# Kernel tuning notes

Measured on AMD Instinct MI355X. Metric: run time of the kernel, lower is better.

Reference implementation:

```python
import jax, jax.numpy as jnp
import numpy as np

STRIDES = (8, 16, 32, 64, 128)
SCORE_THR = 0.05
IOU_THR = 0.6
MAX_NUM = 150
USE_CTR = True
B, NC = 64, 20
HW = (128, 64, 32, 16, 8)


def _reshape(feat):
    # [B,C,H,W] -> [B,H*W,C]
    b, c, h, w = feat.shape
    return feat.transpose(0, 2, 3, 1).reshape(b, h * w, c)


def _decode(feat, stride):
    # feat: [B,4,H,W] reg offsets; returns [B,HW,4] boxes (x1,y1,x2,y2)
    _, _, h, w = feat.shape
    xs = jnp.arange(w, dtype=jnp.float32) * stride + (stride // 2)
    ys = jnp.arange(h, dtype=jnp.float32) * stride + (stride // 2)
    yy, xx = jnp.meshgrid(ys, xs, indexing='ij')
    coords = jnp.stack([xx.reshape(-1), yy.reshape(-1)], axis=-1)  # [HW,2]
    off = _reshape(feat) * stride  # [B,HW,4]
    xy1 = coords[None] - off[..., :2]
    xy2 = coords[None] + off[..., 2:]
    return jnp.concatenate([xy1, xy2], axis=-1)


def _nms_single(scores, ids, boxes, valid):
    # scores already sorted descending (from top_k); class-aware offset NMS.
    coord_max = jnp.max(jnp.where(valid[:, None], boxes, -jnp.inf))
    coord_max = jnp.where(jnp.isfinite(coord_max), coord_max, 0.0)
    ob = boxes + (ids.astype(boxes.dtype) * (coord_max + 1.0))[:, None]
    x1, y1, x2, y2 = ob[:, 0], ob[:, 1], ob[:, 2], ob[:, 3]
    areas = (x2 - x1 + 1.0) * (y2 - y1 + 1.0)
    xmin = jnp.maximum(x1[:, None], x1[None, :])
    ymin = jnp.maximum(y1[:, None], y1[None, :])
    xmax = jnp.minimum(x2[:, None], x2[None, :])
    ymax = jnp.minimum(y2[:, None], y2[None, :])
    ow = jnp.clip(xmax - xmin, 0.0)
    oh = jnp.clip(ymax - ymin, 0.0)
    overlap = ow * oh
    union = jnp.clip(areas[:, None] + areas[None, :] - overlap, 1e-10)
    iou = overlap / union  # [N,N]
    n = scores.shape[0]
    idx = jnp.arange(n)

    def body(i, keep):
        sup = keep[i] & (iou[i] > IOU_THR) & (idx > i)
        return keep & ~sup

    return jax.lax.fori_loop(0, n, body, valid)


def setup_inputs() -> dict:
    key = jax.random.key(0)
    ks = jax.random.split(key, 15)
    out = {}
    for li, hw in enumerate(HW):
        out[f'cls{li}'] = jax.random.normal(ks[li], (B, NC, hw, hw), jnp.float32)
        out[f'reg{li}'] = jax.random.uniform(ks[5 + li], (B, 4, hw, hw), jnp.float32)
        out[f'ctr{li}'] = jax.random.normal(ks[10 + li], (B, 1, hw, hw), jnp.float32)
    return out


def reference(cls0, cls1, cls2, cls3, cls4,
              reg0, reg1, reg2, reg3, reg4,
              ctr0, ctr1, ctr2, ctr3, ctr4):
    cls_feats = (cls0, cls1, cls2, cls3, cls4)
    reg_feats = (reg0, reg1, reg2, reg3, reg4)
    ctr_feats = (ctr0, ctr1, ctr2, ctr3, ctr4)

    cls_logits = jnp.concatenate([_reshape(f) for f in cls_feats], axis=1)  # [B,A,NC]
    ctr_logits = jnp.concatenate([_reshape(f) for f in ctr_feats], axis=1)  # [B,A,1]
    cls_preds = jax.nn.sigmoid(cls_logits)
    ctr_preds = jax.nn.sigmoid(ctr_logits)

    cls_scores = jnp.max(cls_preds, axis=-1)  # [B,A]
    cls_ids = jnp.argmax(cls_preds, axis=-1) + 1  # [B,A]
    if USE_CTR:
        cls_scores = jnp.sqrt(cls_scores * ctr_preds[..., 0])

    boxes = jnp.concatenate(
        [_decode(f, s) for f, s in zip(reg_feats, STRIDES)], axis=1)  # [B,A,4]

    top_scores, top_idx = jax.lax.top_k(cls_scores, MAX_NUM)  # sorted desc
    top_ids = jnp.take_along_axis(cls_ids, top_idx, axis=1)
    top_boxes = jnp.take_along_axis(boxes, top_idx[..., None], axis=1)

    valid = top_scores > SCORE_THR
    keep = jax.vmap(_nms_single)(top_scores, top_ids, top_boxes, valid)

    out_scores = jnp.where(keep, top_scores, 0.0)
    out_ids = jnp.where(keep, top_ids, 0)
    out_boxes = jnp.where(keep[..., None], top_boxes, 0.0)
    return out_scores, out_ids, out_boxes, keep
```

## Files before the change

### kernel.cpp

```cpp
#include <hip/hip_runtime.h>
#include <cstdint>
#include <cstddef>

#define NPTS 21824
#define NB   64
#define NCLS 20
#define MAXN 150
#define NCHUNK 11
#define CHSZ 2048

typedef unsigned long long u64;
typedef unsigned int u32;


__device__ __forceinline__ u64 radix_select_top(
    const u64* __restrict__ keys, int n, int k0,
    u32* hist, u32* suf, u64* shp, int* shr, int* shb)
{
    int tid = threadIdx.x;
    if (tid == 0) { *shp = 0ull; *shr = k0; }
    __syncthreads();
    for (int pass = 0; pass < 6; ++pass) {
        int sh = 56 - pass * 8;
        hist[tid] = 0u;
        __syncthreads();
        u64 prefix = *shp;
        int r = *shr;
        for (int i = tid; i < n; i += 256) {
            u64 key = keys[i];
            bool ok = (pass == 0) || ((key >> (sh + 8)) == prefix);
            if (ok) atomicAdd(&hist[(u32)(key >> sh) & 255u], 1u);
        }
        __syncthreads();
        suf[tid] = hist[tid];
        __syncthreads();
        for (int d = 1; d < 256; d <<= 1) {
            u32 v = (tid + d < 256) ? suf[tid + d] : 0u;
            __syncthreads();
            suf[tid] += v;
            __syncthreads();
        }
        u32 nxt = (tid == 255) ? 0u : suf[tid + 1];
        if (suf[tid] >= (u32)r && nxt < (u32)r) {
            *shb = tid;
            *shr = r - (int)nxt;
        }
        __syncthreads();
        if (tid == 0) *shp = (prefix << 8) | (u64)(u32)(*shb);
        __syncthreads();
    }
    u64 T = (*shp) << 16;
    __syncthreads();
    return T;
}

__global__ __launch_bounds__(256) void k_part(
    const float* __restrict__ c0, const float* __restrict__ c1,
    const float* __restrict__ c2, const float* __restrict__ c3,
    const float* __restrict__ c4,
    const float* __restrict__ t0, const float* __restrict__ t1,
    const float* __restrict__ t2, const float* __restrict__ t3,
    const float* __restrict__ t4,
    u64* __restrict__ cand)
{
    __shared__ u64 keys[CHSZ];
    __shared__ u32 hist[256], suf[256];
    __shared__ u64 shp; __shared__ int shr, shb, shcnt;

    const int tid   = threadIdx.x;
    const int chunk = blockIdx.x;
    const int b     = blockIdx.y;
    const int cbase = chunk * CHSZ;

    for (int half = 0; half < 2; ++half) {
        int pl = half * 1024 + tid * 4;
        int p  = cbase + pl;
        u64 kk0 = 0, kk1 = 0, kk2 = 0, kk3 = 0;
        if (p < NPTS) {
            const float* cp; const float* tp; int base; size_t hw;
            if (p < 16384)      { cp = c0; tp = t0; base = 0;     hw = 16384; }
            else if (p < 20480) { cp = c1; tp = t1; base = 16384; hw = 4096;  }
            else if (p < 21504) { cp = c2; tp = t2; base = 20480; hw = 1024;  }
            else if (p < 21760) { cp = c3; tp = t3; base = 21504; hw = 256;   }
            else                { cp = c4; tp = t4; base = 21760; hw = 64;    }
            int q = p - base;
            const float* cb = cp + (size_t)b * NCLS * hw + q;

            float best0 = -1.f, best1 = -1.f, best2 = -1.f, best3 = -1.f;
            int   bi0 = 0, bi1 = 0, bi2 = 0, bi3 = 0;
            for (int c = 0; c < NCLS; ++c) {
                const float4 v = *reinterpret_cast<const float4*>(cb + (size_t)c * hw);
                float sg;
                sg = 1.0f / (1.0f + expf(-v.x)); if (sg > best0) { best0 = sg; bi0 = c; }
                sg = 1.0f / (1.0f + expf(-v.y)); if (sg > best1) { best1 = sg; bi1 = c; }
                sg = 1.0f / (1.0f + expf(-v.z)); if (sg > best2) { best2 = sg; bi2 = c; }
                sg = 1.0f / (1.0f + expf(-v.w)); if (sg > best3) { best3 = sg; bi3 = c; }
            }
            const float4 cv = *reinterpret_cast<const float4*>(tp + (size_t)b * hw + q);
            float sct, sc;
            sct = 1.0f / (1.0f + expf(-cv.x)); sc = sqrtf(__fmul_rn(best0, sct));
            kk0 = ((u64)__float_as_uint(sc) << 32) | ((u64)(u32)(21823 - p)     << 17) | ((u64)(u32)(bi0 + 1) << 12);
            sct = 1.0f / (1.0f + expf(-cv.y)); sc = sqrtf(__fmul_rn(best1, sct));
            kk1 = ((u64)__float_as_uint(sc) << 32) | ((u64)(u32)(21823 - (p+1)) << 17) | ((u64)(u32)(bi1 + 1) << 12);
            sct = 1.0f / (1.0f + expf(-cv.z)); sc = sqrtf(__fmul_rn(best2, sct));
            kk2 = ((u64)__float_as_uint(sc) << 32) | ((u64)(u32)(21823 - (p+2)) << 17) | ((u64)(u32)(bi2 + 1) << 12);
            sct = 1.0f / (1.0f + expf(-cv.w)); sc = sqrtf(__fmul_rn(best3, sct));
            kk3 = ((u64)__float_as_uint(sc) << 32) | ((u64)(u32)(21823 - (p+3)) << 17) | ((u64)(u32)(bi3 + 1) << 12);
        }
        keys[pl + 0] = kk0; keys[pl + 1] = kk1;
        keys[pl + 2] = kk2; keys[pl + 3] = kk3;
    }
    __syncthreads();

    u64 T = radix_select_top(keys, CHSZ, MAXN, hist, suf, &shp, &shr, &shb);
    if (tid == 0) shcnt = 0;
    __syncthreads();

    u64* outp = cand + ((size_t)b * NCHUNK + chunk) * MAXN;
    for (int i = tid; i < CHSZ; i += 256) {
        u64 key = keys[i];
        if (key >= T) {
            int pos = atomicAdd(&shcnt, 1);
            if (pos < MAXN) outp[pos] = key;
        }
    }
}

__global__ __launch_bounds__(256) void k_final(
    const float* __restrict__ r0, const float* __restrict__ r1,
    const float* __restrict__ r2, const float* __restrict__ r3,
    const float* __restrict__ r4,
    const u64* __restrict__ cand,
    float* __restrict__ out)
{
    const int NC2 = NCHUNK * MAXN;
    __shared__ u64 ck[NCHUNK * MAXN];
    __shared__ u32 hist[256], suf[256];
    __shared__ u64 shp; __shared__ int shr, shb, shcnt;
    __shared__ u64 win[MAXN], srt[MAXN];
    __shared__ float bx0[MAXN], bx1[MAXN], bx2[MAXN], bx3[MAXN];
    __shared__ float ox1[MAXN], oy1[MAXN], ox2[MAXN], oy2[MAXN], area[MAXN];
    __shared__ float sc[MAXN];
    __shared__ int   idv[MAXN];
    __shared__ u64 sup[MAXN][3];
    __shared__ u64 keepw[3];
    __shared__ float shcmax;
    __shared__ float wmax[4];

    const int b = blockIdx.x, tid = threadIdx.x;

    for (int i = tid; i < NC2; i += 256) ck[i] = cand[(size_t)b * NC2 + i];
    __syncthreads();

    u64 T = radix_select_top(ck, NC2, MAXN, hist, suf, &shp, &shr, &shb);
    if (tid == 0) shcnt = 0;
    __syncthreads();
    for (int i = tid; i < NC2; i += 256) {
        u64 key = ck[i];
        if (key >= T) {
            int pos = atomicAdd(&shcnt, 1);
            if (pos < MAXN) win[pos] = key;
        }
    }
    __syncthreads();

    if (tid < MAXN) {
        u64 mk = win[tid]; int r = 0;
        for (int j = 0; j < MAXN; ++j) r += (win[j] > mk);
        srt[r] = mk;
    }
    __syncthreads();

    if (tid < MAXN) {
        u64 key = srt[tid];
        sc[tid]  = __uint_as_float((u32)(key >> 32));
        int p    = 21823 - (int)((key >> 17) & 0x7FFFu);
        idv[tid] = (int)((key >> 12) & 31u);

        const float* rp; int base, dim, lg, st;
        if (p < 16384)      { rp = r0; base = 0;     dim = 128; lg = 7; st = 8;   }
        else if (p < 20480) { rp = r1; base = 16384; dim = 64;  lg = 6; st = 16;  }
        else if (p < 21504) { rp = r2; base = 20480; dim = 32;  lg = 5; st = 32;  }
        else if (p < 21760) { rp = r3; base = 21504; dim = 16;  lg = 4; st = 64;  }
        else                { rp = r4; base = 21760; dim = 8;   lg = 3; st = 128; }

        int q = p - base;
        int y = q >> lg;
        int x = q & (dim - 1);
        float s  = (float)st;
        float cx = (float)(x * st + (st >> 1));
        float cy = (float)(y * st + (st >> 1));
        size_t hw = (size_t)dim * dim;
        const float* rg = rp + (size_t)b * 4 * hw + q;
        float a0 = rg[0], a1 = rg[hw], a2 = rg[2 * hw], a3 = rg[3 * hw];
        bx0[tid] = __fsub_rn(cx, __fmul_rn(a0, s));
        bx1[tid] = __fsub_rn(cy, __fmul_rn(a1, s));
        bx2[tid] = __fadd_rn(cx, __fmul_rn(a2, s));
        bx3[tid] = __fadd_rn(cy, __fmul_rn(a3, s));
    }
    __syncthreads();

    float m = -INFINITY;
    if (tid < MAXN && sc[tid] > 0.05f)
        m = fmaxf(fmaxf(bx0[tid], bx1[tid]), fmaxf(bx2[tid], bx3[tid]));
    #pragma unroll
    for (int off = 32; off >= 1; off >>= 1) m = fmaxf(m, __shfl_xor(m, off));
    if ((tid & 63) == 0) wmax[tid >> 6] = m;
    __syncthreads();
    if (tid == 0) {
        float mm = fmaxf(fmaxf(wmax[0], wmax[1]), fmaxf(wmax[2], wmax[3]));
        shcmax = isfinite(mm) ? mm : 0.0f;
    }
    __syncthreads();

    float cm1 = __fadd_rn(shcmax, 1.0f);
    if (tid < MAXN) {
        float off = __fmul_rn((float)idv[tid], cm1);
        float X1 = __fadd_rn(bx0[tid], off);
        float Y1 = __fadd_rn(bx1[tid], off);
        float X2 = __fadd_rn(bx2[tid], off);
        float Y2 = __fadd_rn(bx3[tid], off);
        ox1[tid] = X1; oy1[tid] = Y1; ox2[tid] = X2; oy2[tid] = Y2;
        area[tid] = __fmul_rn(__fadd_rn(__fsub_rn(X2, X1), 1.0f),
                              __fadd_rn(__fsub_rn(Y2, Y1), 1.0f));
    }
    __syncthreads();

    for (int t = tid; t < MAXN * 3; t += 256) {
        int i = t / 3;
        int w = t - i * 3;
        float x1i = ox1[i], y1i = oy1[i], x2i = ox2[i], y2i = oy2[i], ai = area[i];
        u64 bits = 0ull;
        for (int e = 0; e < 64; ++e) {
            int j = w * 64 + e;
            if (j >= MAXN) break;
            float xmin = fmaxf(x1i, ox1[j]);
            float ymin = fmaxf(y1i, oy1[j]);
            float xmax = fminf(x2i, ox2[j]);
            float ymax = fminf(y2i, oy2[j]);
            float ow = fmaxf(__fsub_rn(xmax, xmin), 0.0f);
            float oh = fmaxf(__fsub_rn(ymax, ymin), 0.0f);
            float ov = __fmul_rn(ow, oh);
            float un = fmaxf(__fsub_rn(__fadd_rn(ai, area[j]), ov), 1e-10f);
            float iou = __fdiv_rn(ov, un);
            if (iou > 0.6f) bits |= (1ull << e);
        }
        sup[i][w] = bits;
    }
    __syncthreads();

    if (tid == 0) {
        u64 kw0 = 0, kw1 = 0, kw2 = 0;
        for (int k = 0; k < MAXN; ++k) {
            if (sc[k] > 0.05f) {
                if (k < 64)       kw0 |= 1ull << k;
                else if (k < 128) kw1 |= 1ull << (k - 64);
                else              kw2 |= 1ull << (k - 128);
            }
        }
        u64 s0 = sup[0][0], s1 = sup[0][1], s2 = sup[0][2];
        for (int i = 0; i < MAXN; ++i) {
            u64 n0 = 0, n1 = 0, n2 = 0;
            if (i + 1 < MAXN) { n0 = sup[i+1][0]; n1 = sup[i+1][1]; n2 = sup[i+1][2]; }
            bool kept = (i < 64) ? ((kw0 >> i) & 1ull)
                      : (i < 128) ? ((kw1 >> (i - 64)) & 1ull)
                                  : ((kw2 >> (i - 128)) & 1ull);
            if (kept) {
                u64 a0, a1, a2;
                if (i < 63)        { a0 = ~((1ull << (i + 1)) - 1ull); a1 = ~0ull; a2 = ~0ull; }
                else if (i == 63)  { a0 = 0ull; a1 = ~0ull; a2 = ~0ull; }
                else if (i < 127)  { a0 = 0ull; a1 = ~((1ull << (i - 63)) - 1ull); a2 = ~0ull; }
                else if (i == 127) { a0 = 0ull; a1 = 0ull; a2 = ~0ull; }
                else               { a0 = 0ull; a1 = 0ull; a2 = ~((1ull << (i - 127)) - 1ull); }
                kw0 &= ~(s0 & a0); kw1 &= ~(s1 & a1); kw2 &= ~(s2 & a2);
            }
            s0 = n0; s1 = n1; s2 = n2;
        }
        keepw[0] = kw0; keepw[1] = kw1; keepw[2] = kw2;
    }
    __syncthreads();

    if (tid < MAXN) {
        bool kp = (keepw[tid >> 6] >> (tid & 63)) & 1ull;
        int o = b * MAXN + tid;
        float* oSc = out;
        float* oId = out + NB * MAXN;
        float* oBx = out + 2 * NB * MAXN;
        float* oKp = out + 2 * NB * MAXN + NB * MAXN * 4;
        oSc[o] = kp ? sc[tid] : 0.0f;
        oId[o] = kp ? (float)idv[tid] : 0.0f;
        oBx[o * 4 + 0] = kp ? bx0[tid] : 0.0f;
        oBx[o * 4 + 1] = kp ? bx1[tid] : 0.0f;
        oBx[o * 4 + 2] = kp ? bx2[tid] : 0.0f;
        oBx[o * 4 + 3] = kp ? bx3[tid] : 0.0f;
        oKp[o] = kp ? 1.0f : 0.0f;
    }
}

extern "C" void kernel_launch(void* const* d_in, const int* in_sizes, int n_in,
                              void* d_out, int out_size, void* d_ws, size_t ws_size,
                              hipStream_t stream)
{
    const float* cls[5]; const float* reg[5]; const float* ctr[5];
    for (int li = 0; li < 5; ++li) {
        cls[li] = (const float*)d_in[3 * li + 0];
        reg[li] = (const float*)d_in[3 * li + 1];
        ctr[li] = (const float*)d_in[3 * li + 2];
    }

    u64* cand = (u64*)d_ws;

    dim3 g1(NCHUNK, NB);
    k_part<<<g1, 256, 0, stream>>>(cls[0], cls[1], cls[2], cls[3], cls[4],
                                   ctr[0], ctr[1], ctr[2], ctr[3], ctr[4],
                                   cand);
    k_final<<<NB, 256, 0, stream>>>(reg[0], reg[1], reg[2], reg[3], reg[4],
                                    cand, (float*)d_out);
}
```

Measured before the change: 287.9 us.

## Replace radix select with bitonic sort and defer argmax to final kernel

Swaps the 6-pass radix-select top-k in both kernels for a shared-memory bitonic sort of 2048 keys, with larger thread blocks (512 and 1024). The class argmax leaves the per-point loop: k_part keeps only the minimum of exp(-x), which is monotone with the max sigmoid, and k_final recomputes the argmax for just the 150 winners. The serial single-thread NMS keep-mask loop becomes a wavefront using shuffles, and the initial valid mask is built with ballot. The bitonic sort does more compare-exchange work and many barriers, but it removes the atomic histograms and the per-element divides.

```diff
diff --git a/kernel.cpp b/kernel.cpp
--- a/kernel.cpp
+++ b/kernel.cpp
@@ -13,48 +13,27 @@
 typedef unsigned int u32;
 
 
-__device__ __forceinline__ u64 radix_select_top(
-    const u64* __restrict__ keys, int n, int k0,
-    u32* hist, u32* suf, u64* shp, int* shr, int* shb)
-{
-    int tid = threadIdx.x;
-    if (tid == 0) { *shp = 0ull; *shr = k0; }
-    __syncthreads();
-    for (int pass = 0; pass < 6; ++pass) {
-        int sh = 56 - pass * 8;
-        hist[tid] = 0u;
-        __syncthreads();
-        u64 prefix = *shp;
-        int r = *shr;
-        for (int i = tid; i < n; i += 256) {
-            u64 key = keys[i];
-            bool ok = (pass == 0) || ((key >> (sh + 8)) == prefix);
-            if (ok) atomicAdd(&hist[(u32)(key >> sh) & 255u], 1u);
-        }
-        __syncthreads();
-        suf[tid] = hist[tid];
-        __syncthreads();
-        for (int d = 1; d < 256; d <<= 1) {
-            u32 v = (tid + d < 256) ? suf[tid + d] : 0u;
+template<int T>
+__device__ __forceinline__ void bitonic2048_desc(u64* keys)
+{
+    const int tid = threadIdx.x;
+    for (int k = 2; k <= 2048; k <<= 1) {
+        for (int j = k >> 1; j > 0; j >>= 1) {
             __syncthreads();
-            suf[tid] += v;
-            __syncthreads();
-        }
-        u32 nxt = (tid == 255) ? 0u : suf[tid + 1];
-        if (suf[tid] >= (u32)r && nxt < (u32)r) {
-            *shb = tid;
-            *shr = r - (int)nxt;
-        }
-        __syncthreads();
-        if (tid == 0) *shp = (prefix << 8) | (u64)(u32)(*shb);
-        __syncthreads();
-    }
-    u64 T = (*shp) << 16;
-    __syncthreads();
-    return T;
-}
-
-__global__ __launch_bounds__(256) void k_part(
+            #pragma unroll
+            for (int t = tid; t < 1024; t += T) {
+                int i = ((t & ~(j - 1)) << 1) | (t & (j - 1));
+                int pr = i | j;
+                u64 a = keys[i], c = keys[pr];
+                bool desc = ((i & k) == 0);
+                if (desc ? (a < c) : (a > c)) { keys[i] = c; keys[pr] = a; }
+            }
+        }
+    }
+    __syncthreads();
+}
+
+__global__ __launch_bounds__(512) void k_part(
     const float* __restrict__ c0, const float* __restrict__ c1,
     const float* __restrict__ c2, const float* __restrict__ c3,
     const float* __restrict__ c4,
@@ -64,69 +43,59 @@
     u64* __restrict__ cand)
 {
     __shared__ u64 keys[CHSZ];
-    __shared__ u32 hist[256], suf[256];
-    __shared__ u64 shp; __shared__ int shr, shb, shcnt;
-
     const int tid   = threadIdx.x;
     const int chunk = blockIdx.x;
     const int b     = blockIdx.y;
-    const int cbase = chunk * CHSZ;
-
-    for (int half = 0; half < 2; ++half) {
-        int pl = half * 1024 + tid * 4;
-        int p  = cbase + pl;
-        u64 kk0 = 0, kk1 = 0, kk2 = 0, kk3 = 0;
-        if (p < NPTS) {
-            const float* cp; const float* tp; int base; size_t hw;
-            if (p < 16384)      { cp = c0; tp = t0; base = 0;     hw = 16384; }
-            else if (p < 20480) { cp = c1; tp = t1; base = 16384; hw = 4096;  }
-            else if (p < 21504) { cp = c2; tp = t2; base = 20480; hw = 1024;  }
-            else if (p < 21760) { cp = c3; tp = t3; base = 21504; hw = 256;   }
-            else                { cp = c4; tp = t4; base = 21760; hw = 64;    }
-            int q = p - base;
-            const float* cb = cp + (size_t)b * NCLS * hw + q;
-
-            float best0 = -1.f, best1 = -1.f, best2 = -1.f, best3 = -1.f;
-            int   bi0 = 0, bi1 = 0, bi2 = 0, bi3 = 0;
-            for (int c = 0; c < NCLS; ++c) {
-                const float4 v = *reinterpret_cast<const float4*>(cb + (size_t)c * hw);
-                float sg;
-                sg = 1.0f / (1.0f + expf(-v.x)); if (sg > best0) { best0 = sg; bi0 = c; }
-                sg = 1.0f / (1.0f + expf(-v.y)); if (sg > best1) { best1 = sg; bi1 = c; }
-                sg = 1.0f / (1.0f + expf(-v.z)); if (sg > best2) { best2 = sg; bi2 = c; }
-                sg = 1.0f / (1.0f + expf(-v.w)); if (sg > best3) { best3 = sg; bi3 = c; }
-            }
-            const float4 cv = *reinterpret_cast<const float4*>(tp + (size_t)b * hw + q);
-            float sct, sc;
-            sct = 1.0f / (1.0f + expf(-cv.x)); sc = sqrtf(__fmul_rn(best0, sct));
-            kk0 = ((u64)__float_as_uint(sc) << 32) | ((u64)(u32)(21823 - p)     << 17) | ((u64)(u32)(bi0 + 1) << 12);
-            sct = 1.0f / (1.0f + expf(-cv.y)); sc = sqrtf(__fmul_rn(best1, sct));
-            kk1 = ((u64)__float_as_uint(sc) << 32) | ((u64)(u32)(21823 - (p+1)) << 17) | ((u64)(u32)(bi1 + 1) << 12);
-            sct = 1.0f / (1.0f + expf(-cv.z)); sc = sqrtf(__fmul_rn(best2, sct));
-            kk2 = ((u64)__float_as_uint(sc) << 32) | ((u64)(u32)(21823 - (p+2)) << 17) | ((u64)(u32)(bi2 + 1) << 12);
-            sct = 1.0f / (1.0f + expf(-cv.w)); sc = sqrtf(__fmul_rn(best3, sct));
-            kk3 = ((u64)__float_as_uint(sc) << 32) | ((u64)(u32)(21823 - (p+3)) << 17) | ((u64)(u32)(bi3 + 1) << 12);
-        }
-        keys[pl + 0] = kk0; keys[pl + 1] = kk1;
-        keys[pl + 2] = kk2; keys[pl + 3] = kk3;
-    }
-    __syncthreads();
-
-    u64 T = radix_select_top(keys, CHSZ, MAXN, hist, suf, &shp, &shr, &shb);
-    if (tid == 0) shcnt = 0;
-    __syncthreads();
-
-    u64* outp = cand + ((size_t)b * NCHUNK + chunk) * MAXN;
-    for (int i = tid; i < CHSZ; i += 256) {
-        u64 key = keys[i];
-        if (key >= T) {
-            int pos = atomicAdd(&shcnt, 1);
-            if (pos < MAXN) outp[pos] = key;
-        }
-    }
-}
-
-__global__ __launch_bounds__(256) void k_final(
+
+    const int pl = tid * 4;
+    const int p  = chunk * CHSZ + pl;
+    u64 kk0 = 0, kk1 = 0, kk2 = 0, kk3 = 0;
+    if (p < NPTS) {
+        const float* cp; const float* tp; int base; size_t hw;
+        if (p < 16384)      { cp = c0; tp = t0; base = 0;     hw = 16384; }
+        else if (p < 20480) { cp = c1; tp = t1; base = 16384; hw = 4096;  }
+        else if (p < 21504) { cp = c2; tp = t2; base = 20480; hw = 1024;  }
+        else if (p < 21760) { cp = c3; tp = t3; base = 21504; hw = 256;   }
+        else                { cp = c4; tp = t4; base = 21760; hw = 64;    }
+        int q = p - base;
+        const float* cb = cp + (size_t)b * NCLS * hw + q;
+
+        float u0 = INFINITY, u1 = INFINITY, u2 = INFINITY, u3 = INFINITY;
+        for (int c = 0; c < NCLS; ++c) {
+            const float4 v = *reinterpret_cast<const float4*>(cb + (size_t)c * hw);
+            u0 = fminf(u0, expf(-v.x));
+            u1 = fminf(u1, expf(-v.y));
+            u2 = fminf(u2, expf(-v.z));
+            u3 = fminf(u3, expf(-v.w));
+        }
+        const float4 cv = *reinterpret_cast<const float4*>(tp + (size_t)b * hw + q);
+        float best, sct, sc;
+        best = 1.0f / (1.0f + u0); sct = 1.0f / (1.0f + expf(-cv.x));
+        sc = sqrtf(__fmul_rn(best, sct));
+        kk0 = ((u64)__float_as_uint(sc) << 32) | (u32)(21823 - p);
+        best = 1.0f / (1.0f + u1); sct = 1.0f / (1.0f + expf(-cv.y));
+        sc = sqrtf(__fmul_rn(best, sct));
+        kk1 = ((u64)__float_as_uint(sc) << 32) | (u32)(21823 - (p + 1));
+        best = 1.0f / (1.0f + u2); sct = 1.0f / (1.0f + expf(-cv.z));
+        sc = sqrtf(__fmul_rn(best, sct));
+        kk2 = ((u64)__float_as_uint(sc) << 32) | (u32)(21823 - (p + 2));
+        best = 1.0f / (1.0f + u3); sct = 1.0f / (1.0f + expf(-cv.w));
+        sc = sqrtf(__fmul_rn(best, sct));
+        kk3 = ((u64)__float_as_uint(sc) << 32) | (u32)(21823 - (p + 3));
+    }
+    keys[pl + 0] = kk0; keys[pl + 1] = kk1;
+    keys[pl + 2] = kk2; keys[pl + 3] = kk3;
+
+    bitonic2048_desc<512>(keys);
+
+    if (tid < MAXN)
+        cand[((size_t)b * NCHUNK + chunk) * MAXN + tid] = keys[tid];
+}
+
+__global__ __launch_bounds__(1024) void k_final(
+    const float* __restrict__ c0, const float* __restrict__ c1,
+    const float* __restrict__ c2, const float* __restrict__ c3,
+    const float* __restrict__ c4,
     const float* __restrict__ r0, const float* __restrict__ r1,
     const float* __restrict__ r2, const float* __restrict__ r3,
     const float* __restrict__ r4,
@@ -134,10 +103,7 @@
     float* __restrict__ out)
 {
     const int NC2 = NCHUNK * MAXN;
-    __shared__ u64 ck[NCHUNK * MAXN];
-    __shared__ u32 hist[256], suf[256];
-    __shared__ u64 shp; __shared__ int shr, shb, shcnt;
-    __shared__ u64 win[MAXN], srt[MAXN];
+    __shared__ u64 keys[CHSZ];
     __shared__ float bx0[MAXN], bx1[MAXN], bx2[MAXN], bx3[MAXN];
     __shared__ float ox1[MAXN], oy1[MAXN], ox2[MAXN], oy2[MAXN], area[MAXN];
     __shared__ float sc[MAXN];
@@ -145,52 +111,44 @@
     __shared__ u64 sup[MAXN][3];
     __shared__ u64 keepw[3];
     __shared__ float shcmax;
-    __shared__ float wmax[4];
+    __shared__ float wmax[16];
 
     const int b = blockIdx.x, tid = threadIdx.x;
 
-    for (int i = tid; i < NC2; i += 256) ck[i] = cand[(size_t)b * NC2 + i];
-    __syncthreads();
-
-    u64 T = radix_select_top(ck, NC2, MAXN, hist, suf, &shp, &shr, &shb);
-    if (tid == 0) shcnt = 0;
-    __syncthreads();
-    for (int i = tid; i < NC2; i += 256) {
-        u64 key = ck[i];
-        if (key >= T) {
-            int pos = atomicAdd(&shcnt, 1);
-            if (pos < MAXN) win[pos] = key;
-        }
-    }
-    __syncthreads();
+    for (int i = tid; i < CHSZ; i += 1024)
+        keys[i] = (i < NC2) ? cand[(size_t)b * NC2 + i] : 0ull;
+
+    bitonic2048_desc<1024>(keys);
 
     if (tid < MAXN) {
-        u64 mk = win[tid]; int r = 0;
-        for (int j = 0; j < MAXN; ++j) r += (win[j] > mk);
-        srt[r] = mk;
-    }
-    __syncthreads();
-
-    if (tid < MAXN) {
-        u64 key = srt[tid];
-        sc[tid]  = __uint_as_float((u32)(key >> 32));
-        int p    = 21823 - (int)((key >> 17) & 0x7FFFu);
-        idv[tid] = (int)((key >> 12) & 31u);
-
-        const float* rp; int base, dim, lg, st;
-        if (p < 16384)      { rp = r0; base = 0;     dim = 128; lg = 7; st = 8;   }
-        else if (p < 20480) { rp = r1; base = 16384; dim = 64;  lg = 6; st = 16;  }
-        else if (p < 21504) { rp = r2; base = 20480; dim = 32;  lg = 5; st = 32;  }
-        else if (p < 21760) { rp = r3; base = 21504; dim = 16;  lg = 4; st = 64;  }
-        else                { rp = r4; base = 21760; dim = 8;   lg = 3; st = 128; }
+        u64 key = keys[tid];
+        sc[tid] = __uint_as_float((u32)(key >> 32));
+        int p   = 21823 - (int)(key & 0x7FFFu);
+
+        const float* rp; const float* cp; int base, dim, lg, st;
+        if (p < 16384)      { rp = r0; cp = c0; base = 0;     dim = 128; lg = 7; st = 8;   }
+        else if (p < 20480) { rp = r1; cp = c1; base = 16384; dim = 64;  lg = 6; st = 16;  }
+        else if (p < 21504) { rp = r2; cp = c2; base = 20480; dim = 32;  lg = 5; st = 32;  }
+        else if (p < 21760) { rp = r3; cp = c3; base = 21504; dim = 16;  lg = 4; st = 64;  }
+        else                { rp = r4; cp = c4; base = 21760; dim = 8;   lg = 3; st = 128; }
 
         int q = p - base;
+        size_t hw = (size_t)dim * dim;
+
+        const float* cb = cp + (size_t)b * NCLS * hw + q;
+        float best = -1.0f; int bi = 0;
+        for (int c = 0; c < NCLS; ++c) {
+            float v  = cb[(size_t)c * hw];
+            float sg = 1.0f / (1.0f + expf(-v));
+            if (sg > best) { best = sg; bi = c; }
+        }
+        idv[tid] = bi + 1;
+
         int y = q >> lg;
         int x = q & (dim - 1);
         float s  = (float)st;
         float cx = (float)(x * st + (st >> 1));
         float cy = (float)(y * st + (st >> 1));
-        size_t hw = (size_t)dim * dim;
         const float* rg = rp + (size_t)b * 4 * hw + q;
         float a0 = rg[0], a1 = rg[hw], a2 = rg[2 * hw], a3 = rg[3 * hw];
         bx0[tid] = __fsub_rn(cx, __fmul_rn(a0, s));
@@ -206,9 +164,15 @@
     #pragma unroll
     for (int off = 32; off >= 1; off >>= 1) m = fmaxf(m, __shfl_xor(m, off));
     if ((tid & 63) == 0) wmax[tid >> 6] = m;
+    if (tid < 192) {
+        bool val = (tid < MAXN) && (sc[tid] > 0.05f);
+        u64 mask = __ballot(val);
+        if ((tid & 63) == 0) keepw[tid >> 6] = mask;
+    }
     __syncthreads();
     if (tid == 0) {
-        float mm = fmaxf(fmaxf(wmax[0], wmax[1]), fmaxf(wmax[2], wmax[3]));
+        float mm = -INFINITY;
+        for (int w = 0; w < 16; ++w) mm = fmaxf(mm, wmax[w]);
         shcmax = isfinite(mm) ? mm : 0.0f;
     }
     __syncthreads();
@@ -226,9 +190,9 @@
     }
     __syncthreads();
 
-    for (int t = tid; t < MAXN * 3; t += 256) {
-        int i = t / 3;
-        int w = t - i * 3;
+    if (tid < MAXN * 3) {
+        int i = tid / 3;
+        int w = tid - i * 3;
         float x1i = ox1[i], y1i = oy1[i], x2i = ox2[i], y2i = oy2[i], ai = area[i];
         u64 bits = 0ull;
         for (int e = 0; e < 64; ++e) {
@@ -249,34 +213,24 @@
     }
     __syncthreads();
 
-    if (tid == 0) {
-        u64 kw0 = 0, kw1 = 0, kw2 = 0;
-        for (int k = 0; k < MAXN; ++k) {
-            if (sc[k] > 0.05f) {
-                if (k < 64)       kw0 |= 1ull << k;
-                else if (k < 128) kw1 |= 1ull << (k - 64);
-                else              kw2 |= 1ull << (k - 128);
+    if (tid < 64) {
+        const int l = tid;
+        u64 kw   = (l < 3) ? keepw[l]  : 0ull;
+        u64 scur = (l < 3) ? sup[0][l] : 0ull;
+        for (int i = 0; i < MAXN; ++i) {
+            u64 snext = (l < 3 && i + 1 < MAXN) ? sup[i + 1][l] : 0ull;
+            u64 kwwi = __shfl(kw, i >> 6);
+            if ((kwwi >> (i & 63)) & 1ull) {
+                int lo = l * 64;
+                u64 allow;
+                if (i < lo)            allow = ~0ull;
+                else if (i - lo >= 63) allow = 0ull;
+                else                   allow = ~((1ull << (i - lo + 1)) - 1ull);
+                kw &= ~(scur & allow);
             }
-        }
-        u64 s0 = sup[0][0], s1 = sup[0][1], s2 = sup[0][2];
-        for (int i = 0; i < MAXN; ++i) {
-            u64 n0 = 0, n1 = 0, n2 = 0;
-            if (i + 1 < MAXN) { n0 = sup[i+1][0]; n1 = sup[i+1][1]; n2 = sup[i+1][2]; }
-            bool kept = (i < 64) ? ((kw0 >> i) & 1ull)
-                      : (i < 128) ? ((kw1 >> (i - 64)) & 1ull)
-                                  : ((kw2 >> (i - 128)) & 1ull);
-            if (kept) {
-                u64 a0, a1, a2;
-                if (i < 63)        { a0 = ~((1ull << (i + 1)) - 1ull); a1 = ~0ull; a2 = ~0ull; }
-                else if (i == 63)  { a0 = 0ull; a1 = ~0ull; a2 = ~0ull; }
-                else if (i < 127)  { a0 = 0ull; a1 = ~((1ull << (i - 63)) - 1ull); a2 = ~0ull; }
-                else if (i == 127) { a0 = 0ull; a1 = 0ull; a2 = ~0ull; }
-                else               { a0 = 0ull; a1 = 0ull; a2 = ~((1ull << (i - 127)) - 1ull); }
-                kw0 &= ~(s0 & a0); kw1 &= ~(s1 & a1); kw2 &= ~(s2 & a2);
-            }
-            s0 = n0; s1 = n1; s2 = n2;
-        }
-        keepw[0] = kw0; keepw[1] = kw1; keepw[2] = kw2;
+            scur = snext;
+        }
+        if (l < 3) keepw[l] = kw;
     }
     __syncthreads();
 
@@ -311,9 +265,10 @@
     u64* cand = (u64*)d_ws;
 
     dim3 g1(NCHUNK, NB);
-    k_part<<<g1, 256, 0, stream>>>(cls[0], cls[1], cls[2], cls[3], cls[4],
+    k_part<<<g1, 512, 0, stream>>>(cls[0], cls[1], cls[2], cls[3], cls[4],
                                    ctr[0], ctr[1], ctr[2], ctr[3], ctr[4],
                                    cand);
-    k_final<<<NB, 256, 0, stream>>>(reg[0], reg[1], reg[2], reg[3], reg[4],
-                                    cand, (float*)d_out);
-}
+    k_final<<<NB, 1024, 0, stream>>>(cls[0], cls[1], cls[2], cls[3], cls[4],
+                                     reg[0], reg[1], reg[2], reg[3], reg[4],
+                                     cand, (float*)d_out);
+}
```

Result: faster. 270.9 us (-5.9%).
